# Kernel tuning notes

Measured on AMD Instinct MI355X. Metric: run time of the kernel, lower is better.

The kernel has to match this reference:

```python
import jax, jax.numpy as jnp
import numpy as np

B, C, W, H = 4, 256, 64, 64
DK = C // 8  # query/key channels


def setup_inputs() -> dict:
    key = jax.random.key(0)
    ks = jax.random.split(key, 7)
    x = jax.random.normal(ks[0], (B, C, W, H), dtype=jnp.float32)
    # conv1x1 weights stored as [out_ch, in_ch]
    Wq = jax.random.normal(ks[1], (DK, C), dtype=jnp.float32) / np.sqrt(C)
    bq = jnp.zeros((DK,), dtype=jnp.float32)
    Wk = jax.random.normal(ks[2], (DK, C), dtype=jnp.float32) / np.sqrt(C)
    bk = jnp.zeros((DK,), dtype=jnp.float32)
    Wv = jax.random.normal(ks[3], (C, C), dtype=jnp.float32) / np.sqrt(C)
    bv = jnp.zeros((C,), dtype=jnp.float32)
    gamma = jnp.zeros((1,), dtype=jnp.float32)
    return {"x": x, "Wq": Wq, "bq": bq, "Wk": Wk, "bk": bk,
            "Wv": Wv, "bv": bv, "gamma": gamma}


def reference(x, Wq, bq, Wk, bk, Wv, bv, gamma):
    b, c, w, h = x.shape
    n = w * h
    xf = x.reshape(b, c, n)                     # [B, C, N]
    # conv1x1 == channel matmul
    q = jnp.einsum('dc,bcn->bnd', Wq, xf) + bq  # [B, N, DK]
    k = jnp.einsum('dc,bcn->bdn', Wk, xf) + bk[None, :, None]  # [B, DK, N]
    energy = jnp.einsum('bnd,bdm->bnm', q, k)   # [B, N, N]
    attention = jax.nn.softmax(energy, axis=-1)
    v = jnp.einsum('dc,bcn->bdn', Wv, xf) + bv[None, :, None]  # [B, C, N]
    out = jnp.einsum('bdm,bnm->bdn', v, attention)              # [B, C, N]
    out = out.reshape(b, c, w, h)
    out = gamma * out + x
    return out, attention
```

## Files before the change

kernel.cpp:

```cpp
#include <hip/hip_runtime.h>
#include <hip/hip_bf16.h>

typedef __attribute__((ext_vector_type(8))) short bf16x8;
typedef __attribute__((ext_vector_type(4))) float f32x4;
typedef __attribute__((ext_vector_type(4))) unsigned int u32x4;
typedef __attribute__((ext_vector_type(2))) unsigned int u32x2;

#define B_SZ 4
#define C_SZ 256
#define N_SZ 4096
#define DK_SZ 32

#define WQB_OFF 0
#define WKB_OFF 8192
#define WVB_OFF 16384
#define QB_OFF  81920
#define KB_OFF  606208
#define VB_OFF  1130496

__device__ __forceinline__ short f2bf(float f) {
    union { float f; unsigned int u; } v; v.f = f;
    unsigned int r = v.u + 0x7fffu + ((v.u >> 16) & 1u);
    return (short)(r >> 16);
}

__device__ __forceinline__ unsigned int cvt_pk_bf16(float lo, float hi) {
    unsigned int r;
    asm volatile("v_cvt_pk_bf16_f32 %0, %1, %2" : "=v"(r) : "v"(lo), "v"(hi));
    return r;
}

__device__ __forceinline__ f32x4 mfma16(bf16x8 a, bf16x8 b, f32x4 c) {
    return __builtin_amdgcn_mfma_f32_16x16x32_bf16(a, b, c, 0, 0, 0);
}

__device__ __forceinline__ void gload_lds16(const void* g, void* l) {
    __builtin_amdgcn_global_load_lds((const __attribute__((address_space(1))) unsigned int*)g,
                                     (__attribute__((address_space(3))) unsigned int*)l, 16, 0, 0);
}

__global__ __launch_bounds__(256) void k_convw(const float* __restrict__ Wq,
                                               const float* __restrict__ Wk,
                                               const float* __restrict__ Wv,
                                               short* __restrict__ ws) {
    int i = blockIdx.x * 256 + threadIdx.x;
    if (i < 8192) {
        ws[WQB_OFF + i] = f2bf(Wq[i]);
        ws[WKB_OFF + i] = f2bf(Wk[i]);
    }
    ws[WVB_OFF + i] = f2bf(Wv[i]);
}

__global__ __launch_bounds__(256) void k_prep(const float* __restrict__ x,
                                              const float* __restrict__ bq,
                                              const float* __restrict__ bk,
                                              const float* __restrict__ bv,
                                              short* __restrict__ ws) {
    __shared__ short xsT[64][264];
    __shared__ short vt_s[64][258];

    const int b = blockIdx.y;
    const int n0 = blockIdx.x * 64;
    const int t = threadIdx.x;
    const float* xb = x + (size_t)b * C_SZ * N_SZ;

    {
        int c0 = t >> 4, n4 = (t & 15) * 4;
#pragma unroll
        for (int i = 0; i < 16; i++) {
            int c = c0 + 16 * i;
            float4 v = *(const float4*)(xb + (size_t)c * N_SZ + n0 + n4);
            xsT[n4 + 0][c] = f2bf(v.x);
            xsT[n4 + 1][c] = f2bf(v.y);
            xsT[n4 + 2][c] = f2bf(v.z);
            xsT[n4 + 3][c] = f2bf(v.w);
        }
    }
    __syncthreads();

    const int w = t >> 6, l = t & 63;
    const int lr = l & 15, lk = l >> 4;

    bf16x8 af[8];
#pragma unroll
    for (int kk = 0; kk < 8; kk++)
        af[kk] = *(const bf16x8*)(&xsT[w * 16 + lr][kk * 32 + lk * 8]);

#pragma unroll
    for (int qk = 0; qk < 2; qk++) {
        const short* wb = ws + (qk ? WKB_OFF : WQB_OFF);
        const float* bias = qk ? bk : bq;
        short* outp = ws + (qk ? KB_OFF : QB_OFF) + (size_t)b * N_SZ * DK_SZ;
#pragma unroll
        for (int cf = 0; cf < 2; cf++) {
            f32x4 acc = {0.f, 0.f, 0.f, 0.f};
#pragma unroll
            for (int kk = 0; kk < 8; kk++) {
                bf16x8 bfr = *(const bf16x8*)(wb + (cf * 16 + lr) * 256 + kk * 32 + lk * 8);
                acc = mfma16(af[kk], bfr, acc);
            }
            float bias_v = bias[cf * 16 + lr];
#pragma unroll
            for (int r = 0; r < 4; r++) {
                int row = w * 16 + lk * 4 + r;
                outp[(size_t)(n0 + row) * DK_SZ + cf * 16 + lr] = f2bf(acc[r] + bias_v);
            }
        }
    }

#pragma unroll
    for (int cf = 0; cf < 16; cf++) {
        f32x4 acc = {0.f, 0.f, 0.f, 0.f};
#pragma unroll
        for (int kk = 0; kk < 8; kk++) {
            bf16x8 bfr = *(const bf16x8*)(ws + WVB_OFF + (cf * 16 + lr) * 256 + kk * 32 + lk * 8);
            acc = mfma16(af[kk], bfr, acc);
        }
        float bias_v = bv[cf * 16 + lr];
#pragma unroll
        for (int r = 0; r < 4; r++) {
            vt_s[w * 16 + lk * 4 + r][cf * 16 + lr] = f2bf(acc[r] + bias_v);
        }
    }
    __syncthreads();
    {
        short* vb = ws + VB_OFF + (size_t)b * C_SZ * N_SZ;
        int nn = t & 63;
#pragma unroll
        for (int i = 0; i < 64; i++) {
            int c = (t >> 6) + 4 * i;
            vb[(size_t)c * N_SZ + n0 + nn] = vt_s[nn][c];
        }
    }
}

__global__ __launch_bounds__(512, 1) void k_attn(const short* __restrict__ ws,
                                                 const float* __restrict__ x,
                                                 const float* __restrict__ gamma_p,
                                                 float* __restrict__ out) {
    __shared__ short v_lds[2][256 * 64];
    __shared__ short p_lds[2][64][72];
    __shared__ float rsum_s[2][64];

    const int b = blockIdx.y;
    const int n0 = blockIdx.x * 64;
    const int t = threadIdx.x, w = t >> 6, l = t & 63;
    const int rg = w & 3, ch = w >> 2;
    const int lr = l & 15, lk = l >> 4;

    const short* qb = ws + QB_OFF + (size_t)b * N_SZ * DK_SZ;
    const short* kb = ws + KB_OFF + (size_t)b * N_SZ * DK_SZ;
    const short* vb = ws + VB_OFF + (size_t)b * C_SZ * N_SZ;

    bf16x8 qf = *(const bf16x8*)(qb + (size_t)(n0 + rg * 16 + lr) * DK_SZ + lk * 8);

    float rs = 0.f;
    for (int mt = 0; mt < 32; mt++) {
        int mb = ch * 2048 + mt * 64;
        bf16x8 kf0 = *(const bf16x8*)(kb + (size_t)(mb + lr) * DK_SZ + lk * 8);
        bf16x8 kf1 = *(const bf16x8*)(kb + (size_t)(mb + 16 + lr) * DK_SZ + lk * 8);
        bf16x8 kf2 = *(const bf16x8*)(kb + (size_t)(mb + 32 + lr) * DK_SZ + lk * 8);
        bf16x8 kf3 = *(const bf16x8*)(kb + (size_t)(mb + 48 + lr) * DK_SZ + lk * 8);
        f32x4 s0 = mfma16(kf0, qf, (f32x4){0.f, 0.f, 0.f, 0.f});
        f32x4 s1 = mfma16(kf1, qf, (f32x4){0.f, 0.f, 0.f, 0.f});
        f32x4 s2 = mfma16(kf2, qf, (f32x4){0.f, 0.f, 0.f, 0.f});
        f32x4 s3 = mfma16(kf3, qf, (f32x4){0.f, 0.f, 0.f, 0.f});
#pragma unroll
        for (int r = 0; r < 4; r++)
            rs += __expf(s0[r]) + __expf(s1[r]) + __expf(s2[r]) + __expf(s3[r]);
    }
    rs += __shfl_xor(rs, 16);
    rs += __shfl_xor(rs, 32);
    if (l < 16) rsum_s[ch][rg * 16 + l] = rs;
    __syncthreads();
    const float invp = 1.f / (rsum_s[0][rg * 16 + lr] + rsum_s[1][rg * 16 + lr]);

    float* attn = out + (size_t)B_SZ * C_SZ * N_SZ + (size_t)b * N_SZ * N_SZ;
    f32x4 O[8];
#pragma unroll
    for (int cb = 0; cb < 8; cb++) O[cb] = (f32x4){0.f, 0.f, 0.f, 0.f};

#define SPRIME(tt, pb)                                                                   \
    {                                                                                    \
        int mbase = (tt) * 64 + ch * 32;                                                 \
        _Pragma("unroll")                                                                \
        for (int t16 = 0; t16 < 2; t16++) {                                              \
            bf16x8 kf = *(const bf16x8*)(kb + (size_t)(mbase + t16 * 16 + lr) * DK_SZ + lk * 8); \
            f32x4 s = mfma16(kf, qf, (f32x4){0.f, 0.f, 0.f, 0.f});                       \
            float4 e;                                                                    \
            e.x = __expf(s[0]) * invp; e.y = __expf(s[1]) * invp;                        \
            e.z = __expf(s[2]) * invp; e.w = __expf(s[3]) * invp;                        \
            *(float4*)(attn + (size_t)(n0 + rg * 16 + lr) * N_SZ + mbase + t16 * 16 + lk * 4) = e; \
            u32x2 pk;                                                                    \
            pk[0] = cvt_pk_bf16(e.x, e.y);                                               \
            pk[1] = cvt_pk_bf16(e.z, e.w);                                               \
            *(u32x2*)(&p_lds[pb][rg * 16 + lr][ch * 32 + t16 * 16 + lk * 4]) = pk;       \
        }                                                                                \
    }

#define STAGE(tt, vbuf)                                                                  \
    {                                                                                    \
        int mb = (tt) * 64;                                                              \
        _Pragma("unroll")                                                                \
        for (int i = 0; i < 4; i++) {                                                    \
            int c = w * 32 + i * 8 + (l >> 3);                                           \
            int j = l & 7;                                                               \
            const short* g = vb + (size_t)c * N_SZ + mb + ((j ^ (c & 7)) << 3);          \
            gload_lds16(g, (void*)&v_lds[vbuf][(w * 32 + i * 8) * 64]);                  \
        }                                                                                \
    }

    STAGE(0, 0);
    SPRIME(0, 0);

    for (int mt = 0; mt < 64; mt++) {
        __syncthreads();
        int cur = mt & 1;
        if (mt < 63) {
            STAGE(mt + 1, cur ^ 1);
            SPRIME(mt + 1, cur ^ 1);
        }
        const char* pbase = (const char*)&p_lds[cur][rg * 16 + lr][0];
        bf16x8 pa0 = *(const bf16x8*)(pbase + lk * 16);
        bf16x8 pa1 = *(const bf16x8*)(pbase + 64 + lk * 16);
        const char* vbase = (const char*)&v_lds[cur][0];
#pragma unroll
        for (int cb = 0; cb < 8; cb++) {
            int c = ch * 128 + cb * 16 + lr;
            int sw = (c & 7) << 4;
            bf16x8 b0 = *(const bf16x8*)(vbase + c * 128 + ((lk << 4) ^ sw));
            bf16x8 b1 = *(const bf16x8*)(vbase + c * 128 + (((4 + lk) << 4) ^ sw));
            O[cb] = mfma16(pa0, b0, O[cb]);
            O[cb] = mfma16(pa1, b1, O[cb]);
        }
    }

    __syncthreads();
    const float g = gamma_p[0];
    float* o_s = (float*)&v_lds[0][0];
    const float* xb = x + (size_t)b * C_SZ * N_SZ;
    float* ob = out + (size_t)b * C_SZ * N_SZ;
#pragma unroll
    for (int half = 0; half < 2; half++) {
        if ((rg >> 1) == half) {
#pragma unroll
            for (int cb = 0; cb < 8; cb++) {
#pragma unroll
                for (int r = 0; r < 4; r++) {
                    o_s[((rg & 1) * 16 + lk * 4 + r) * 258 + ch * 128 + cb * 16 + lr] = O[cb][r];
                }
            }
        }
        __syncthreads();
        {
            int nn = t & 31;
            int c0 = t >> 5;
#pragma unroll
            for (int i = 0; i < 16; i++) {
                int c = c0 + 16 * i;
                size_t idx = (size_t)c * N_SZ + n0 + half * 32 + nn;
                ob[idx] = g * o_s[nn * 258 + c] + xb[idx];
            }
        }
        __syncthreads();
    }
}

extern "C" void kernel_launch(void* const* d_in, const int* in_sizes, int n_in,
                              void* d_out, int out_size, void* d_ws, size_t ws_size,
                              hipStream_t stream) {
    const float* x     = (const float*)d_in[0];
    const float* Wq    = (const float*)d_in[1];
    const float* bq    = (const float*)d_in[2];
    const float* Wk    = (const float*)d_in[3];
    const float* bk    = (const float*)d_in[4];
    const float* Wv    = (const float*)d_in[5];
    const float* bv    = (const float*)d_in[6];
    const float* gamma = (const float*)d_in[7];
    short* ws = (short*)d_ws;
    float* out = (float*)d_out;

    hipLaunchKernelGGL(k_convw, dim3(256), dim3(256), 0, stream, Wq, Wk, Wv, ws);
    hipLaunchKernelGGL(k_prep, dim3(64, 4), dim3(256), 0, stream, x, bq, bk, bv, ws);
    hipLaunchKernelGGL(k_attn, dim3(64, 4), dim3(512), 0, stream, ws, x, gamma, out);
}
```

Baseline: 166.0 us.

## Triple-buffer V tiles, retile PV MFMA per wave, use nontemporal attention stores

The PV loop moves from double to triple-buffered V staging, prefetching two tiles ahead, and replaces the per-iteration __syncthreads with an explicit s_waitcnt plus s_barrier under sched_barrier fences. K fragments for the next tile are loaded separately from the softmax compute so load latency overlaps work. Each wave now computes a 2x4 block of output tiles instead of 1x8, so each V fragment read from LDS feeds two MFMAs. Attention probabilities are written with nontemporal stores to limit cache pollution. The costs are more LDS for the third V buffer and reliance on hand-counted vmcnt values for correctness.

```diff
diff --git a/kernel.cpp b/kernel.cpp
--- a/kernel.cpp
+++ b/kernel.cpp
@@ -134,11 +134,11 @@
     }
 }
 
-__global__ __launch_bounds__(512, 1) void k_attn(const short* __restrict__ ws,
+__global__ __launch_bounds__(512, 2) void k_attn(const short* __restrict__ ws,
                                                  const float* __restrict__ x,
                                                  const float* __restrict__ gamma_p,
                                                  float* __restrict__ out) {
-    __shared__ short v_lds[2][256 * 64];
+    __shared__ short v_lds[3][256 * 64];
     __shared__ short p_lds[2][64][72];
     __shared__ float rsum_s[2][64];
 
@@ -146,6 +146,7 @@
     const int n0 = blockIdx.x * 64;
     const int t = threadIdx.x, w = t >> 6, l = t & 63;
     const int rg = w & 3, ch = w >> 2;
+    const int rp = w & 1, cp = w >> 1;
     const int lr = l & 15, lk = l >> 4;
 
     const short* qb = ws + QB_OFF + (size_t)b * N_SZ * DK_SZ;
@@ -157,14 +158,14 @@
     float rs = 0.f;
     for (int mt = 0; mt < 32; mt++) {
         int mb = ch * 2048 + mt * 64;
-        bf16x8 kf0 = *(const bf16x8*)(kb + (size_t)(mb + lr) * DK_SZ + lk * 8);
-        bf16x8 kf1 = *(const bf16x8*)(kb + (size_t)(mb + 16 + lr) * DK_SZ + lk * 8);
-        bf16x8 kf2 = *(const bf16x8*)(kb + (size_t)(mb + 32 + lr) * DK_SZ + lk * 8);
-        bf16x8 kf3 = *(const bf16x8*)(kb + (size_t)(mb + 48 + lr) * DK_SZ + lk * 8);
-        f32x4 s0 = mfma16(kf0, qf, (f32x4){0.f, 0.f, 0.f, 0.f});
-        f32x4 s1 = mfma16(kf1, qf, (f32x4){0.f, 0.f, 0.f, 0.f});
-        f32x4 s2 = mfma16(kf2, qf, (f32x4){0.f, 0.f, 0.f, 0.f});
-        f32x4 s3 = mfma16(kf3, qf, (f32x4){0.f, 0.f, 0.f, 0.f});
+        bf16x8 kfa = *(const bf16x8*)(kb + (size_t)(mb + lr) * DK_SZ + lk * 8);
+        bf16x8 kfb = *(const bf16x8*)(kb + (size_t)(mb + 16 + lr) * DK_SZ + lk * 8);
+        bf16x8 kfc = *(const bf16x8*)(kb + (size_t)(mb + 32 + lr) * DK_SZ + lk * 8);
+        bf16x8 kfd = *(const bf16x8*)(kb + (size_t)(mb + 48 + lr) * DK_SZ + lk * 8);
+        f32x4 s0 = mfma16(kfa, qf, (f32x4){0.f, 0.f, 0.f, 0.f});
+        f32x4 s1 = mfma16(kfb, qf, (f32x4){0.f, 0.f, 0.f, 0.f});
+        f32x4 s2 = mfma16(kfc, qf, (f32x4){0.f, 0.f, 0.f, 0.f});
+        f32x4 s3 = mfma16(kfd, qf, (f32x4){0.f, 0.f, 0.f, 0.f});
 #pragma unroll
         for (int r = 0; r < 4; r++)
             rs += __expf(s0[r]) + __expf(s1[r]) + __expf(s2[r]) + __expf(s3[r]);
@@ -175,65 +176,96 @@
     __syncthreads();
     const float invp = 1.f / (rsum_s[0][rg * 16 + lr] + rsum_s[1][rg * 16 + lr]);
 
-    float* attn = out + (size_t)B_SZ * C_SZ * N_SZ + (size_t)b * N_SZ * N_SZ;
-    f32x4 O[8];
-#pragma unroll
-    for (int cb = 0; cb < 8; cb++) O[cb] = (f32x4){0.f, 0.f, 0.f, 0.f};
-
-#define SPRIME(tt, pb)                                                                   \
-    {                                                                                    \
-        int mbase = (tt) * 64 + ch * 32;                                                 \
-        _Pragma("unroll")                                                                \
-        for (int t16 = 0; t16 < 2; t16++) {                                              \
-            bf16x8 kf = *(const bf16x8*)(kb + (size_t)(mbase + t16 * 16 + lr) * DK_SZ + lk * 8); \
-            f32x4 s = mfma16(kf, qf, (f32x4){0.f, 0.f, 0.f, 0.f});                       \
-            float4 e;                                                                    \
-            e.x = __expf(s[0]) * invp; e.y = __expf(s[1]) * invp;                        \
-            e.z = __expf(s[2]) * invp; e.w = __expf(s[3]) * invp;                        \
-            *(float4*)(attn + (size_t)(n0 + rg * 16 + lr) * N_SZ + mbase + t16 * 16 + lk * 4) = e; \
-            u32x2 pk;                                                                    \
-            pk[0] = cvt_pk_bf16(e.x, e.y);                                               \
-            pk[1] = cvt_pk_bf16(e.z, e.w);                                               \
-            *(u32x2*)(&p_lds[pb][rg * 16 + lr][ch * 32 + t16 * 16 + lk * 4]) = pk;       \
-        }                                                                                \
-    }
-
-#define STAGE(tt, vbuf)                                                                  \
-    {                                                                                    \
-        int mb = (tt) * 64;                                                              \
-        _Pragma("unroll")                                                                \
-        for (int i = 0; i < 4; i++) {                                                    \
-            int c = w * 32 + i * 8 + (l >> 3);                                           \
-            int j = l & 7;                                                               \
-            const short* g = vb + (size_t)c * N_SZ + mb + ((j ^ (c & 7)) << 3);          \
-            gload_lds16(g, (void*)&v_lds[vbuf][(w * 32 + i * 8) * 64]);                  \
-        }                                                                                \
-    }
-
+    float* attn_row = out + (size_t)B_SZ * C_SZ * N_SZ + (size_t)b * N_SZ * N_SZ
+                      + (size_t)(n0 + rg * 16 + lr) * N_SZ;
+    f32x4 O[2][4];
+#pragma unroll
+    for (int rf = 0; rf < 2; rf++)
+#pragma unroll
+        for (int cb = 0; cb < 4; cb++) O[rf][cb] = (f32x4){0.f, 0.f, 0.f, 0.f};
+
+    bf16x8 kf0, kf1;
+
+#define KLOAD(tt)                                                                  \
+    {                                                                              \
+        const int mbase = (tt) * 64 + ch * 32;                                     \
+        kf0 = *(const bf16x8*)(kb + (size_t)(mbase + lr) * DK_SZ + lk * 8);        \
+        kf1 = *(const bf16x8*)(kb + (size_t)(mbase + 16 + lr) * DK_SZ + lk * 8);   \
+    }
+
+#define STAGE(tt, vbuf)                                                            \
+    {                                                                              \
+        const int mb = (tt) * 64;                                                  \
+        _Pragma("unroll")                                                          \
+        for (int i = 0; i < 4; i++) {                                              \
+            int c = w * 32 + i * 8 + (l >> 3);                                     \
+            int j = l & 7;                                                         \
+            const short* g = vb + (size_t)c * N_SZ + mb + ((j ^ (c & 7)) << 3);    \
+            gload_lds16(g, (void*)&v_lds[vbuf][(w * 32 + i * 8) * 64]);            \
+        }                                                                          \
+    }
+
+#define SCOMP(tt, pb)                                                              \
+    {                                                                              \
+        const int mbase = (tt) * 64 + ch * 32;                                     \
+        f32x4 s0 = mfma16(kf0, qf, (f32x4){0.f, 0.f, 0.f, 0.f});                   \
+        f32x4 s1 = mfma16(kf1, qf, (f32x4){0.f, 0.f, 0.f, 0.f});                   \
+        f32x4 e0, e1;                                                              \
+        e0[0] = __expf(s0[0]) * invp; e0[1] = __expf(s0[1]) * invp;                \
+        e0[2] = __expf(s0[2]) * invp; e0[3] = __expf(s0[3]) * invp;                \
+        e1[0] = __expf(s1[0]) * invp; e1[1] = __expf(s1[1]) * invp;                \
+        e1[2] = __expf(s1[2]) * invp; e1[3] = __expf(s1[3]) * invp;                \
+        __builtin_nontemporal_store(e0, (f32x4*)(attn_row + mbase + lk * 4));      \
+        __builtin_nontemporal_store(e1, (f32x4*)(attn_row + mbase + 16 + lk * 4)); \
+        u32x2 pk0, pk1;                                                            \
+        pk0[0] = cvt_pk_bf16(e0[0], e0[1]); pk0[1] = cvt_pk_bf16(e0[2], e0[3]);    \
+        pk1[0] = cvt_pk_bf16(e1[0], e1[1]); pk1[1] = cvt_pk_bf16(e1[2], e1[3]);    \
+        *(u32x2*)(&p_lds[pb][rg * 16 + lr][ch * 32 + lk * 4]) = pk0;               \
+        *(u32x2*)(&p_lds[pb][rg * 16 + lr][ch * 32 + 16 + lk * 4]) = pk1;          \
+    }
+
+    KLOAD(0);
+    __builtin_amdgcn_sched_barrier(0);
     STAGE(0, 0);
-    SPRIME(0, 0);
+    STAGE(1, 1);
+    __builtin_amdgcn_sched_barrier(0);
+    SCOMP(0, 0);
 
     for (int mt = 0; mt < 64; mt++) {
-        __syncthreads();
-        int cur = mt & 1;
+        asm volatile("s_waitcnt vmcnt(6) lgkmcnt(0)" ::: "memory");
+        __builtin_amdgcn_sched_barrier(0);
+        __builtin_amdgcn_s_barrier();
+        __builtin_amdgcn_sched_barrier(0);
+        const int cur = mt & 1;
         if (mt < 63) {
-            STAGE(mt + 1, cur ^ 1);
-            SPRIME(mt + 1, cur ^ 1);
-        }
-        const char* pbase = (const char*)&p_lds[cur][rg * 16 + lr][0];
-        bf16x8 pa0 = *(const bf16x8*)(pbase + lk * 16);
-        bf16x8 pa1 = *(const bf16x8*)(pbase + 64 + lk * 16);
-        const char* vbase = (const char*)&v_lds[cur][0];
-#pragma unroll
-        for (int cb = 0; cb < 8; cb++) {
-            int c = ch * 128 + cb * 16 + lr;
+            KLOAD(mt + 1);
+            __builtin_amdgcn_sched_barrier(0);
+            if (mt < 62) STAGE(mt + 2, (mt + 2) % 3);
+            __builtin_amdgcn_sched_barrier(0);
+            SCOMP(mt + 1, cur ^ 1);
+        }
+        const int vcur = mt % 3;
+        const char* pbase = (const char*)&p_lds[cur][rp * 32 + lr][0];
+        bf16x8 a00 = *(const bf16x8*)(pbase + lk * 16);
+        bf16x8 a01 = *(const bf16x8*)(pbase + 64 + lk * 16);
+        bf16x8 a10 = *(const bf16x8*)(pbase + 2304 + lk * 16);
+        bf16x8 a11 = *(const bf16x8*)(pbase + 2304 + 64 + lk * 16);
+        const char* vbase = (const char*)&v_lds[vcur][0];
+#pragma unroll
+        for (int cb = 0; cb < 4; cb++) {
+            int c = cp * 64 + cb * 16 + lr;
             int sw = (c & 7) << 4;
             bf16x8 b0 = *(const bf16x8*)(vbase + c * 128 + ((lk << 4) ^ sw));
             bf16x8 b1 = *(const bf16x8*)(vbase + c * 128 + (((4 + lk) << 4) ^ sw));
-            O[cb] = mfma16(pa0, b0, O[cb]);
-            O[cb] = mfma16(pa1, b1, O[cb]);
-        }
-    }
+            O[0][cb] = mfma16(a00, b0, O[0][cb]);
+            O[0][cb] = mfma16(a01, b1, O[0][cb]);
+            O[1][cb] = mfma16(a10, b0, O[1][cb]);
+            O[1][cb] = mfma16(a11, b1, O[1][cb]);
+        }
+    }
+#undef KLOAD
+#undef STAGE
+#undef SCOMP
 
     __syncthreads();
     const float g = gamma_p[0];
@@ -242,14 +274,14 @@
     float* ob = out + (size_t)b * C_SZ * N_SZ;
 #pragma unroll
     for (int half = 0; half < 2; half++) {
-        if ((rg >> 1) == half) {
-#pragma unroll
-            for (int cb = 0; cb < 8; cb++) {
-#pragma unroll
-                for (int r = 0; r < 4; r++) {
-                    o_s[((rg & 1) * 16 + lk * 4 + r) * 258 + ch * 128 + cb * 16 + lr] = O[cb][r];
-                }
-            }
+        if (rp == half) {
+#pragma unroll
+            for (int rf = 0; rf < 2; rf++)
+#pragma unroll
+                for (int cb = 0; cb < 4; cb++)
+#pragma unroll
+                    for (int r = 0; r < 4; r++)
+                        o_s[(rf * 16 + lk * 4 + r) * 258 + cp * 64 + cb * 16 + lr] = O[rf][cb][r];
         }
         __syncthreads();
         {
```

Result: faster. 155.3 us (-6.4%).
